# Kernel optimization log

Measured on AMD Instinct MI355X. Metric: run time of the kernel, lower is better.

Reference implementation:

```python
import jax, jax.numpy as jnp
import numpy as np

N_HEAD = 8
D_MODEL = 512


def setup_inputs() -> dict:
    key = jax.random.key(0)
    ks = jax.random.split(key, 9)
    B, S, D, H = 4, 1024, D_MODEL, N_HEAD
    s = 1.0 / np.sqrt(D)
    return {
        "x": jax.random.normal(ks[0], (B, S, D), dtype=jnp.float32),
        "Wq": jax.random.normal(ks[1], (D, H * D), dtype=jnp.float32) * s,
        "bq": jnp.zeros((H * D,), jnp.float32),
        "Wk": jax.random.normal(ks[2], (D, H * D), dtype=jnp.float32) * s,
        "bk": jnp.zeros((H * D,), jnp.float32),
        "Wv": jax.random.normal(ks[3], (D, H * D), dtype=jnp.float32) * s,
        "bv": jnp.zeros((H * D,), jnp.float32),
        "Wo": jax.random.normal(ks[4], (H * D, D), dtype=jnp.float32) * (1.0 / np.sqrt(H * D)),
        "bo": jnp.zeros((D,), jnp.float32),
    }


def reference(x, Wq, bq, Wk, bk, Wv, bv, Wo, bo):
    B, S, D = x.shape
    H = N_HEAD
    # QKV projections, split into heads: [B, S, H, D] (each head uses full d_model)
    q = (x @ Wq + bq).reshape(B, S, H, D)
    k = (x @ Wk + bk).reshape(B, S, H, D)
    v = (x @ Wv + bv).reshape(B, S, H, D)
    # scores: [H, B, Sq, Sk], scaled by 1/d_model (scale=d_model in original)
    scores = jnp.einsum("bqhd,bkhd->hbqk", q, k) / D
    attn = jax.nn.softmax(scores, axis=-1)
    # context: [B, Sq, H, D] -> concat heads -> output projection
    ctx = jnp.einsum("hbqk,bkhd->bqhd", attn, v).reshape(B, S, H * D)
    out = ctx @ Wo + bo
    # attn returned as [(H*B), Sq, Sk] matching torch head-major layout
    return out, attn.reshape(H * B, S, S)
```

## Files before the change

### kernel.cpp

```cpp
#include <hip/hip_runtime.h>
#include <hip/hip_bf16.h>


typedef unsigned short u16;
typedef __attribute__((ext_vector_type(8))) short short8;
typedef __attribute__((ext_vector_type(4))) float f32x4;
typedef __attribute__((ext_vector_type(2))) unsigned int u32x2;

#define BK 32

__device__ __forceinline__ u16 f2bf(float f) {
    union { float f; unsigned u; } v; v.f = f;
    unsigned u = v.u;
    u += 0x7fffu + ((u >> 16) & 1u);
    return (u16)(u >> 16);
}

__device__ __forceinline__ void gl2lds16(const void* g, void* l) {
    __builtin_amdgcn_global_load_lds(
        (const __attribute__((address_space(1))) void*)g,
        (__attribute__((address_space(3))) void*)l, 16, 0, 0);
}

template<int MF, int NF, bool AF32, bool OUTF32, bool ROWBIAS, bool DBUF>
__global__ __launch_bounds__(256)
void gemm_bt(const void* __restrict__ Ap, int lda, long long sAh, long long sAb,
             const u16* __restrict__ Bp, int ldb, long long sBh, long long sBb,
             void* __restrict__ Cp, int ldc, long long sCh, long long sCb,
             int K, const float* __restrict__ bias, long long sbias,
             float scale, int nb)
{
    constexpr int BMt = MF * 32, BNt = NF * 32;
    constexpr int AW = AF32 ? 2 * BK : BK;
    constexpr int NB = DBUF ? 2 : 1;
    __shared__ __attribute__((aligned(16))) u16 Alds[NB][BMt][AW];
    __shared__ __attribute__((aligned(16))) u16 Blds[NB][BNt][BK];

    int bx = blockIdx.x, by = blockIdx.y, bz = blockIdx.z;
    {
        const int gx = gridDim.x, gy = gridDim.y;
        const int nwg = gx * gy * (int)gridDim.z;
        const int wgid = bx + gx * (by + gy * bz);
        const int xcd = wgid & 7, lp = wgid >> 3;
        const int q = nwg >> 3, r = nwg & 7;
        int nid = (xcd < r ? xcd * (q + 1) : r * (q + 1) + (xcd - r) * q) + lp;
        bx = nid % gx; nid /= gx; by = nid % gy; bz = nid / gy;
    }

    const int zh = bz / nb, zb = bz % nb;
    const int m0 = by * BMt;
    const int n0 = bx * BNt;

    const int tid  = threadIdx.x;
    const int lane = tid & 63;
    const int wave = tid >> 6;
    const int wm = (wave >> 1) * (MF * 16);
    const int wn = (wave & 1) * (NF * 16);

    const float* Afp = (const float*)Ap + (long long)zh * sAh + (long long)zb * sAb;
    const u16*   Abf = (const u16*)Ap + (long long)zh * sAh + (long long)zb * sAb;
    const u16*   Bbf = Bp + (long long)zh * sBh + (long long)zb * sBb;

    f32x4 acc[MF][NF] = {};

    auto stage = [&](int buf, int kt) {
        if (AF32) {
            #pragma unroll
            for (int i = 0; i < BMt / 32; ++i) {
                int idx = i * 256 + tid;
                int row = idx >> 3;
                int c   = idx & 7;
                int cs  = c ^ (row & 7);
                gl2lds16(Afp + (long long)(m0 + row) * lda + kt + (cs << 2),
                         (u16*)&Alds[buf][0][0] + idx * 8);
            }
        } else {
            #pragma unroll
            for (int i = 0; i < BMt / 64; ++i) {
                int idx = i * 256 + tid;
                int row = idx >> 2;
                int kq  = (idx & 3) << 3;
                gl2lds16(Abf + (long long)(m0 + row) * lda + (kt + kq),
                         &Alds[buf][row][kq]);
            }
        }
        #pragma unroll
        for (int i = 0; i < BNt / 64; ++i) {
            int idx = i * 256 + tid;
            int row = idx >> 2;
            int kq  = (idx & 3) << 3;
            gl2lds16(Bbf + (long long)(n0 + row) * ldb + (kt + kq),
                     &Blds[buf][row][kq]);
        }
    };

    auto compute = [&](int buf) {
        const int kq = (lane >> 4) << 3;
        const int fr = lane & 15;
        short8 af[MF], bfr[NF];
        if (AF32) {
            const int c0 = (lane >> 4) << 1;
            #pragma unroll
            for (int im = 0; im < MF; ++im) {
                int row = wm + im * 16 + fr;
                int s   = row & 7;
                const float* ar = (const float*)&Alds[buf][row][0];
                f32x4 lo = *(const f32x4*)(ar + (((c0    ) ^ s) << 2));
                f32x4 hi = *(const f32x4*)(ar + (((c0 + 1) ^ s) << 2));
                union { short8 v; __hip_bfloat162 h[4]; } a;
                a.h[0] = __float22bfloat162_rn(make_float2(lo.x, lo.y));
                a.h[1] = __float22bfloat162_rn(make_float2(lo.z, lo.w));
                a.h[2] = __float22bfloat162_rn(make_float2(hi.x, hi.y));
                a.h[3] = __float22bfloat162_rn(make_float2(hi.z, hi.w));
                af[im] = a.v;
            }
        } else {
            #pragma unroll
            for (int im = 0; im < MF; ++im)
                af[im] = *(const short8*)(&Alds[buf][wm + im * 16 + fr][kq]);
        }
        #pragma unroll
        for (int in = 0; in < NF; ++in)
            bfr[in] = *(const short8*)(&Blds[buf][wn + in * 16 + fr][kq]);
        #pragma unroll
        for (int im = 0; im < MF; ++im)
            #pragma unroll
            for (int in = 0; in < NF; ++in)
                acc[im][in] = __builtin_amdgcn_mfma_f32_16x16x32_bf16(
                    af[im], bfr[in], acc[im][in], 0, 0, 0);
    };

    const int nt = K / BK;
    if (DBUF) {
        stage(0, 0);
        for (int t = 0; t < nt; ++t) {
            const int cur = t & 1;
            __syncthreads();
            if (t + 1 < nt)
                stage(cur ^ 1, (t + 1) * BK);
            compute(cur);
        }
    } else {
        for (int t = 0; t < nt; ++t) {
            __syncthreads();
            stage(0, t * BK);
            __syncthreads();
            compute(0);
        }
    }

    float* Cfp = (float*)Cp + (long long)zh * sCh + (long long)zb * sCb;
    u16*   Cbf = (u16*)Cp + (long long)zh * sCh + (long long)zb * sCb;
    const float* biasp = bias ? bias + (long long)zh * sbias : nullptr;
    const int rb  = (lane >> 4) << 2;
    const int col = lane & 15;
    #pragma unroll
    for (int im = 0; im < MF; ++im) {
        #pragma unroll
        for (int r = 0; r < 4; ++r) {
            int row = m0 + wm + im * 16 + rb + r;
            float rbias = (biasp && ROWBIAS) ? biasp[row] : 0.0f;
            #pragma unroll
            for (int in = 0; in < NF; ++in) {
                int cc = n0 + wn + in * 16 + col;
                float v = acc[im][in][r] * scale;
                if (biasp) v += ROWBIAS ? rbias : biasp[cc];
                if (OUTF32) Cfp[(long long)row * ldc + cc] = v;
                else        Cbf[(long long)row * ldc + cc] = f2bf(v);
            }
        }
    }
}

__global__ __launch_bounds__(256)
void softmax_kernel(float* __restrict__ attn)
{
    const long long row = blockIdx.x;
    float* p = attn + row * 1024;
    const int tid  = threadIdx.x;
    const int lane = tid & 63;
    const int wave = tid >> 6;
    __shared__ float red[8];

    f32x4 v = *(f32x4*)(p + tid * 4);
    float mx = fmaxf(fmaxf(v.x, v.y), fmaxf(v.z, v.w));
    #pragma unroll
    for (int off = 1; off < 64; off <<= 1)
        mx = fmaxf(mx, __shfl_xor(mx, off, 64));
    if (lane == 0) red[wave] = mx;
    __syncthreads();
    mx = fmaxf(fmaxf(red[0], red[1]), fmaxf(red[2], red[3]));

    v.x = __expf(v.x - mx);
    v.y = __expf(v.y - mx);
    v.z = __expf(v.z - mx);
    v.w = __expf(v.w - mx);
    float s = v.x + v.y + v.z + v.w;
    #pragma unroll
    for (int off = 1; off < 64; off <<= 1)
        s += __shfl_xor(s, off, 64);
    if (lane == 0) red[4 + wave] = s;
    __syncthreads();
    s = red[4] + red[5] + red[6] + red[7];
    float inv = 1.0f / s;
    v.x *= inv; v.y *= inv; v.z *= inv; v.w *= inv;
    *(f32x4*)(p + tid * 4) = v;
}

__global__ __launch_bounds__(256)
void cvt_kernel(const float* __restrict__ in, u16* __restrict__ out)
{
    long long i = (long long)blockIdx.x * 256 + threadIdx.x;
    f32x4 v = *(const f32x4*)(in + i * 4);
    u32x2 p;
    p.x = (unsigned)f2bf(v.x) | ((unsigned)f2bf(v.y) << 16);
    p.y = (unsigned)f2bf(v.z) | ((unsigned)f2bf(v.w) << 16);
    *(u32x2*)(out + i * 4) = p;
}

__global__ __launch_bounds__(256)
void wtrans_kernel(const float* __restrict__ in, u16* __restrict__ out, int R, int C)
{
    __shared__ __attribute__((aligned(16))) u16 t[64][72];
    const int r0 = blockIdx.y * 64, c0 = blockIdx.x * 64;
    const int tid = threadIdx.x;
    const int lr = tid >> 4;
    const int lc = (tid & 15) << 2;
    #pragma unroll
    for (int j = 0; j < 4; ++j) {
        int rr = lr + j * 16;
        f32x4 v = *(const f32x4*)(in + (long long)(r0 + rr) * C + c0 + lc);
        u32x2 p;
        p.x = (unsigned)f2bf(v.x) | ((unsigned)f2bf(v.y) << 16);
        p.y = (unsigned)f2bf(v.z) | ((unsigned)f2bf(v.w) << 16);
        *(u32x2*)(&t[rr][lc]) = p;
    }
    __syncthreads();
    const int oc = tid >> 2;
    const int rs = (tid & 3) << 4;
    union { short8 v; u16 e[8]; } a, b;
    #pragma unroll
    for (int j = 0; j < 8; ++j) a.e[j] = t[rs + j][oc];
    #pragma unroll
    for (int j = 0; j < 8; ++j) b.e[j] = t[rs + 8 + j][oc];
    u16* o = out + (long long)(c0 + oc) * R + r0 + rs;
    *(short8*)o = a.v;
    *(short8*)(o + 8) = b.v;
}

extern "C" void kernel_launch(void* const* d_in, const int* in_sizes, int n_in,
                              void* d_out, int out_size, void* d_ws, size_t ws_size,
                              hipStream_t stream)
{
    const float* x  = (const float*)d_in[0];
    const float* Wq = (const float*)d_in[1];
    const float* bq = (const float*)d_in[2];
    const float* Wk = (const float*)d_in[3];
    const float* bk = (const float*)d_in[4];
    const float* Wv = (const float*)d_in[5];
    const float* bv = (const float*)d_in[6];
    const float* Wo = (const float*)d_in[7];
    const float* bo = (const float*)d_in[8];

    const int B = 4, S = 1024, D = 512, H = 8;
    const int HD = H * D;
    const int BS = B * S;

    float* out  = (float*)d_out;
    float* attn = out + (long long)BS * D;

    u16* xb   = (u16*)d_ws;
    u16* WqT  = xb  + (long long)BS * D;
    u16* WkT  = WqT + (long long)HD * D;
    u16* WvT  = WkT + (long long)HD * D;
    u16* WoT  = WvT + (long long)HD * D;
    u16* buf1 = WoT + (long long)D * HD;
    u16* buf2 = buf1 + (long long)BS * HD;

    dim3 blk(256);

    cvt_kernel<<<dim3(BS * D / 1024), blk, 0, stream>>>(x, xb);
    wtrans_kernel<<<dim3(HD / 64, D / 64), blk, 0, stream>>>(Wq, WqT, D, HD);
    wtrans_kernel<<<dim3(HD / 64, D / 64), blk, 0, stream>>>(Wk, WkT, D, HD);
    wtrans_kernel<<<dim3(HD / 64, D / 64), blk, 0, stream>>>(Wv, WvT, D, HD);
    wtrans_kernel<<<dim3(D / 64, HD / 64), blk, 0, stream>>>(Wo, WoT, HD, D);

    {
        dim3 g(HD / 128, BS / 128, 1);
        gemm_bt<4,4,false,false,false,true><<<g, blk, 0, stream>>>(
            xb, D, 0, 0, WqT, D, 0, 0, buf1, HD, 0, 0, D, bq, 0, 1.0f, 1);
        gemm_bt<4,4,false,false,false,true><<<g, blk, 0, stream>>>(
            xb, D, 0, 0, WkT, D, 0, 0, buf2, HD, 0, 0, D, bk, 0, 1.0f, 1);
    }
    {
        dim3 g(S / 128, S / 128, H * B);
        gemm_bt<4,4,false,true,false,true><<<g, blk, 0, stream>>>(
            buf1, HD, D, (long long)S * HD,
            buf2, HD, D, (long long)S * HD,
            attn, S, (long long)B * S * S, (long long)S * S,
            D, nullptr, 0, 1.0f / (float)D, B);
    }
    softmax_kernel<<<dim3(H * B * S), blk, 0, stream>>>(attn);
    {
        dim3 g(S / 128, D / 128, H * B);
        gemm_bt<4,4,false,false,true,true><<<g, blk, 0, stream>>>(
            WvT, D, (long long)D * D, 0,
            xb, D, 0, (long long)S * D,
            buf1, S, (long long)B * D * S, (long long)D * S,
            D, bv, D, 1.0f, B);
    }
    {
        dim3 g(D / 128, S / 128, H * B);
        gemm_bt<4,4,true,false,false,false><<<g, blk, 0, stream>>>(
            attn, S, (long long)B * S * S, (long long)S * S,
            buf1, S, (long long)B * D * S, (long long)D * S,
            buf2, HD, D, (long long)S * HD,
            S, nullptr, 0, 1.0f, B);
    }
    {
        dim3 g(D / 128, BS / 64, 1);
        gemm_bt<2,4,false,true,false,true><<<g, blk, 0, stream>>>(
            buf2, HD, 0, 0, WoT, HD, 0, 0, out, D, 0, 0, HD, bo, 0, 1.0f, 1);
    }
}
```

Baseline: 518.4 us.

## Triple-buffer GEMM LDS staging with vmcnt waits and shrink output-projection tiles

Replaces the double-buffered GEMM main loop with a three-stage LDS pipeline that prefetches two K-tiles ahead. It waits on outstanding global-to-LDS loads with explicit s_waitcnt vmcnt counts and uses a raw s_barrier instead of __syncthreads. The output projection also switches to 64x64 tiles, launching more workgroups for better CU occupancy. This adds LDS usage and relies on the hand-computed vmcnt values matching the number of loads issued per stage.

Measured after the change: 510.9 us. About the same (-1.5%).

```diff
diff --git a/kernel.cpp b/kernel.cpp
--- a/kernel.cpp
+++ b/kernel.cpp
@@ -22,7 +22,7 @@
         (__attribute__((address_space(3))) void*)l, 16, 0, 0);
 }
 
-template<int MF, int NF, bool AF32, bool OUTF32, bool ROWBIAS, bool DBUF>
+template<int MF, int NF, bool AF32, bool OUTF32, bool ROWBIAS, bool PIPE>
 __global__ __launch_bounds__(256)
 void gemm_bt(const void* __restrict__ Ap, int lda, long long sAh, long long sAb,
              const u16* __restrict__ Bp, int ldb, long long sBh, long long sBb,
@@ -30,11 +30,13 @@
              int K, const float* __restrict__ bias, long long sbias,
              float scale, int nb)
 {
+    static_assert(!(PIPE && AF32), "PIPE path assumes bf16 A staging");
     constexpr int BMt = MF * 32, BNt = NF * 32;
     constexpr int AW = AF32 ? 2 * BK : BK;
-    constexpr int NB = DBUF ? 2 : 1;
-    __shared__ __attribute__((aligned(16))) u16 Alds[NB][BMt][AW];
-    __shared__ __attribute__((aligned(16))) u16 Blds[NB][BNt][BK];
+    constexpr int NBUF = PIPE ? 3 : 1;
+    constexpr int LPT = BMt / 64 + BNt / 64;
+    __shared__ __attribute__((aligned(16))) u16 Alds[NBUF][BMt][AW];
+    __shared__ __attribute__((aligned(16))) u16 Blds[NBUF][BNt][BK];
 
     int bx = blockIdx.x, by = blockIdx.y, bz = blockIdx.z;
     {
@@ -131,15 +133,29 @@
     };
 
     const int nt = K / BK;
-    if (DBUF) {
+    if (PIPE) {
         stage(0, 0);
+        stage(1, BK);
         for (int t = 0; t < nt; ++t) {
-            const int cur = t & 1;
-            __syncthreads();
-            if (t + 1 < nt)
-                stage(cur ^ 1, (t + 1) * BK);
-            compute(cur);
-        }
+            if (t < nt - 1) {
+                if constexpr (LPT == 4)
+                    asm volatile("s_waitcnt vmcnt(4)" ::: "memory");
+                else if constexpr (LPT == 3)
+                    asm volatile("s_waitcnt vmcnt(3)" ::: "memory");
+                else if constexpr (LPT == 2)
+                    asm volatile("s_waitcnt vmcnt(2)" ::: "memory");
+                else
+                    asm volatile("s_waitcnt vmcnt(0)" ::: "memory");
+            } else {
+                asm volatile("s_waitcnt vmcnt(0)" ::: "memory");
+            }
+            __builtin_amdgcn_s_barrier();
+            __builtin_amdgcn_sched_barrier(0);
+            const int nx = t + 2;
+            if (nx < nt) stage(nx - nx / 3 * 3, nx * BK);
+            compute(t - t / 3 * 3);
+        }
+        __builtin_amdgcn_s_barrier();
     } else {
         for (int t = 0; t < nt; ++t) {
             __syncthreads();
@@ -318,8 +334,8 @@
             S, nullptr, 0, 1.0f, B);
     }
     {
-        dim3 g(D / 128, BS / 64, 1);
-        gemm_bt<2,4,false,true,false,true><<<g, blk, 0, stream>>>(
+        dim3 g(D / 64, BS / 64, 1);
+        gemm_bt<2,2,false,true,false,true><<<g, blk, 0, stream>>>(
             buf2, HD, 0, 0, WoT, HD, 0, 0, out, D, 0, 0, HD, bo, 0, 1.0f, 1);
     }
 }
```
